# Optimization experiments

Hardware: AMD Instinct MI355X
Metric: run time of the kernel (lower is better)

Reference implementation:

```python
import jax, jax.numpy as jnp
import numpy as np

N, E, H, D_IN, D_EDGE, L = 20000, 320000, 128, 128, 32, 4
EPS = 1e-5

def setup_inputs() -> dict:
    key = jax.random.key(0)
    ks = jax.random.split(key, 16)
    d_in_edge = 2 * H + 1 + D_EDGE  # cat[h_row, h_col, radial, edge_attr] (input_nf==hidden here)
    s = 0.02
    inp = {
        'h': jax.random.normal(ks[0], (N, D_IN), jnp.float32),
        'coords': jax.random.normal(ks[1], (N, 3), jnp.float32),
        'edge_attr': jax.random.normal(ks[2], (E, D_EDGE), jnp.float32),
        'edges': jax.random.randint(ks[3], (2, E), 0, N),
        'edge_w1': jax.random.normal(ks[4], (L, d_in_edge, H), jnp.float32) * s,
        'edge_b1': jnp.zeros((L, H), jnp.float32),
        'edge_w2': jax.random.normal(ks[5], (L, H, H), jnp.float32) * s,
        'edge_b2': jnp.zeros((L, H), jnp.float32),
        'node_w1': jax.random.normal(ks[6], (L, H + H, H), jnp.float32) * s,
        'node_b1': jnp.zeros((L, H), jnp.float32),
        'node_w2': jax.random.normal(ks[7], (L, H, H), jnp.float32) * s,
        'node_b2': jnp.zeros((L, H), jnp.float32),
        'ln_g': jnp.ones((H,), jnp.float32),
        'ln_b': jnp.zeros((H,), jnp.float32),
    }
    return inp

def _egnn(h, coords, edge_attr, edges, ew1, eb1, ew2, eb2, nw1, nb1, nw2, nb2, ln_g, ln_b):
    row, col = edges[0], edges[1]
    # squared-distance radial feature; coords are not updated across layers
    # (EGNN.forward discards coordinate updates: h, _, _ = layer(...)).
    diff = coords[row] - coords[col]              # [E,3]
    radial = jnp.sum(diff * diff, axis=-1, keepdims=True)  # [E,1]
    for i in range(L):
        hr, hc = h[row], h[col]                   # gathers [E,H]
        m = jnp.concatenate([hr, hc, radial, edge_attr], axis=-1)
        m = jax.nn.silu(m @ ew1[i] + eb1[i])      # [E,H]
        m = jax.nn.silu(m @ ew2[i] + eb2[i])      # [E,H]
        agg = jax.ops.segment_sum(m, row, num_segments=N)  # scatter-add [N,H]
        z = jnp.concatenate([h, agg], axis=-1)    # [N,2H]
        out = jax.nn.silu(z @ nw1[i] + nb1[i]) @ nw2[i] + nb2[i]
        h = out if i == 0 else h + out            # layer 0 non-recurrent
    mu = jnp.mean(h, axis=-1, keepdims=True)
    var = jnp.mean((h - mu) ** 2, axis=-1, keepdims=True)
    return (h - mu) * jax.lax.rsqrt(var + EPS) * ln_g + ln_b

def reference(h, coords, edge_attr, edges, edge_w1, edge_b1, edge_w2, edge_b2,
              node_w1, node_b1, node_w2, node_b2, ln_g, ln_b):
    return _egnn(h, coords, edge_attr, edges, edge_w1, edge_b1, edge_w2, edge_b2,
                 node_w1, node_b1, node_w2, node_b2, ln_g, ln_b)
```

## Files before the change

### kernel.cpp

```cpp
#include <hip/hip_runtime.h>
#include <hip/hip_bf16.h>

#define NN 20000
#define EE 320000
#define HH 128
#define DE 32
#define LL 4

typedef __bf16 bf16_t;
typedef __bf16 bf16x8 __attribute__((ext_vector_type(8)));
typedef __bf16 bf16x4 __attribute__((ext_vector_type(4)));
typedef float f32x4 __attribute__((ext_vector_type(4)));

static __device__ __forceinline__ float silu_f(float x) {
    return x * __builtin_amdgcn_rcpf(1.f + __expf(-x));
}

static __device__ __forceinline__ int permrow(int el) {
    return ((el >> 2) & 3) * 16 + ((el >> 4) & 3) * 4 + (el & 3);
}

__global__ void prep_weights(const float* __restrict__ ew1, const float* __restrict__ eb1f,
                             const float* __restrict__ ew2,
                             const float* __restrict__ nw1, const float* __restrict__ nw2,
                             bf16_t* __restrict__ WPT, bf16_t* __restrict__ W1C,
                             bf16_t* __restrict__ W2T, bf16_t* __restrict__ N1T,
                             bf16_t* __restrict__ N2T)
{
    int i = blockIdx.x * 256 + threadIdx.x;
    const int SW = LL * 256 * 128;
    if (i < SW) {
        int l = i / (256 * 128), r = i % (256 * 128);
        int c = r / 128, k = r % 128;
        int krow = (c < 128) ? k : 128 + k;
        WPT[i] = (bf16_t)ew1[((size_t)l * 289 + krow) * 128 + (c & 127)];
        return;
    }
    i -= SW;
    const int SC = LL * 128 * 64;
    if (i < SC) {
        int l = i / (128 * 64), r = i % (128 * 64);
        int c = r / 64, kk = r % 64;
        float v;
        if (kk == 0)       v = ew1[((size_t)l * 289 + 256) * 128 + c];
        else if (kk <= 32) v = ew1[((size_t)l * 289 + 256 + kk) * 128 + c];
        else if (kk == 33) v = eb1f[l * 128 + c];
        else               v = 0.f;
        W1C[i] = (bf16_t)v;
        return;
    }
    i -= SC;
    const int S2 = LL * 128 * 128;
    if (i < S2) {
        int l = i / (128 * 128), r = i % (128 * 128);
        int n = r / 128, k = r % 128;
        W2T[i] = (bf16_t)ew2[((size_t)l * 128 + k) * 128 + n];
        return;
    }
    i -= S2;
    const int S3 = LL * 128 * 256;
    if (i < S3) {
        int l = i / (128 * 256), r = i % (128 * 256);
        int n = r / 256, k = r % 256;
        N1T[i] = (bf16_t)nw1[((size_t)l * 256 + k) * 128 + n];
        return;
    }
    i -= S3;
    if (i < S2) {
        int l = i / (128 * 128), r = i % (128 * 128);
        int n = r / 128, k = r % 128;
        N2T[i] = (bf16_t)nw2[((size_t)l * 128 + k) * 128 + n];
    }
}

__global__ void hist_kernel(const int* __restrict__ edges, int* __restrict__ counts)
{
    int e = blockIdx.x * 256 + threadIdx.x;
    if (e < EE) atomicAdd(&counts[edges[e]], 1);
}

__global__ void scan_kernel(const int* __restrict__ counts, int* __restrict__ starts)
{
    __shared__ int wsum[16];
    __shared__ int running_s;
    const int tid = threadIdx.x;
    const int lane = tid & 63, wv = tid >> 6;
    if (tid == 0) running_s = 0;
    __syncthreads();
    for (int base = 0; base < NN; base += 1024) {
        int i = base + tid;
        int v = (i < NN) ? counts[i] : 0;
        int orig = v;
        #pragma unroll
        for (int off = 1; off < 64; off <<= 1) {
            int t = __shfl_up(v, off);
            if (lane >= off) v += t;
        }
        if (lane == 63) wsum[wv] = v;
        __syncthreads();
        if (tid < 16) {
            int s = wsum[tid];
            #pragma unroll
            for (int off = 1; off < 16; off <<= 1) {
                int t = __shfl_up(s, off);
                if (tid >= off) s += t;
            }
            wsum[tid] = s;
        }
        __syncthreads();
        int waveoff = (wv == 0) ? 0 : wsum[wv - 1];
        if (i < NN) starts[i] = running_s + waveoff + v - orig;
        int total = wsum[15];
        __syncthreads();
        if (tid == 0) running_s += total;
        __syncthreads();
    }
}

__global__ void scatter_kernel(const int* __restrict__ edges, int* __restrict__ cursor,
                               int* __restrict__ eidx, int* __restrict__ row_s,
                               int* __restrict__ col_s)
{
    int e = blockIdx.x * 256 + threadIdx.x;
    if (e >= EE) return;
    int r = edges[e], c = edges[EE + e];
    int pos = atomicAdd(&cursor[r], 1);
    eidx[pos] = e;
    row_s[pos] = r;
    col_s[pos] = c;
}

__global__ void build_re(const int* __restrict__ eidx, const int* __restrict__ row_s,
                         const int* __restrict__ col_s, const float* __restrict__ coords,
                         const float* __restrict__ ea, bf16_t* __restrict__ RE)
{
    int pos = blockIdx.x * 256 + threadIdx.x;
    if (pos >= EE) return;
    int e = eidx[pos], r = row_s[pos], c = col_s[pos];
    float dx = coords[r * 3 + 0] - coords[c * 3 + 0];
    float dy = coords[r * 3 + 1] - coords[c * 3 + 1];
    float dz = coords[r * 3 + 2] - coords[c * 3 + 2];
    alignas(16) bf16_t buf[40];
    buf[0] = (bf16_t)(dx * dx + dy * dy + dz * dz);
    #pragma unroll
    for (int j = 0; j < 32; ++j) buf[1 + j] = (bf16_t)ea[(size_t)e * DE + j];
    buf[33] = (bf16_t)1.0f;
    #pragma unroll
    for (int j = 34; j < 40; ++j) buf[j] = (bf16_t)0.f;
    bf16x8* dst = (bf16x8*)(RE + (size_t)pos * 40);
    #pragma unroll
    for (int k = 0; k < 5; ++k) dst[k] = ((const bf16x8*)buf)[k];
}

__global__ __launch_bounds__(256, 2) void node_pre(
    const float* __restrict__ h, const bf16_t* __restrict__ WPT,
    bf16_t* __restrict__ P, int layer)
{
    __shared__ bf16_t Hs[64][136];
    const int tid = threadIdx.x;
    const int n0 = blockIdx.x * 64;
    {
        const int nl = tid >> 2, q = tid & 3;
        const int node = n0 + nl;
        if (node < NN) {
            const float* hp = h + (size_t)node * HH;
            #pragma unroll
            for (int j = 0; j < 8; ++j) {
                float4 v = *(const float4*)(hp + q * 32 + j * 4);
                int k = q * 32 + j * 4;
                Hs[nl][k + 0] = (bf16_t)v.x; Hs[nl][k + 1] = (bf16_t)v.y;
                Hs[nl][k + 2] = (bf16_t)v.z; Hs[nl][k + 3] = (bf16_t)v.w;
            }
        } else {
            #pragma unroll
            for (int j = 0; j < 8; ++j) {
                int k = q * 32 + j * 4;
                Hs[nl][k] = (bf16_t)0.f; Hs[nl][k + 1] = (bf16_t)0.f;
                Hs[nl][k + 2] = (bf16_t)0.f; Hs[nl][k + 3] = (bf16_t)0.f;
            }
        }
    }
    __syncthreads();

    const int lane = tid & 63, w = tid >> 6;
    const int ln = lane & 15, kg = lane >> 4;

    f32x4 acc[4][4] = {};
    const bf16_t* Wl = WPT + (size_t)layer * 256 * 128;
    #pragma unroll
    for (int kt = 0; kt < 4; ++kt) {
        const int kb = kt * 32 + kg * 8;
        bf16x8 a[4], b[4];
        #pragma unroll
        for (int m = 0; m < 4; ++m) a[m] = *(const bf16x8*)&Hs[m * 16 + ln][kb];
        #pragma unroll
        for (int n = 0; n < 4; ++n)
            b[n] = *(const bf16x8*)(Wl + (size_t)(w * 64 + n * 16 + ln) * 128 + kb);
        #pragma unroll
        for (int m = 0; m < 4; ++m)
            #pragma unroll
            for (int n = 0; n < 4; ++n)
                acc[m][n] = __builtin_amdgcn_mfma_f32_16x16x32_bf16(a[m], b[n], acc[m][n], 0, 0, 0);
    }
    #pragma unroll
    for (int n = 0; n < 4; ++n) {
        int col = w * 64 + n * 16 + ln;
        #pragma unroll
        for (int m = 0; m < 4; ++m)
            #pragma unroll
            for (int rr = 0; rr < 4; ++rr) {
                int node = n0 + m * 16 + kg * 4 + rr;
                if (node < NN) P[(size_t)node * 256 + col] = (bf16_t)acc[m][n][rr];
            }
    }
}

__global__ __launch_bounds__(256, 6) void edge_kernel(
    const bf16_t* __restrict__ P, const bf16_t* __restrict__ RE,
    const int* __restrict__ row_s, const int* __restrict__ col_s,
    const bf16_t* __restrict__ W1C, const bf16_t* __restrict__ W2T,
    const float* __restrict__ b2, float* __restrict__ agg, int layer)
{
    __shared__ bf16_t pABs[64][136];
    __shared__ bf16_t REb[64][72];

    const int tid = threadIdx.x;
    const int e0 = blockIdx.x * 64;

    {
        const int el = tid >> 2, q = tid & 3;
        const int es = e0 + permrow(el);
        const bf16_t* src = RE + (size_t)es * 40;
        bf16x8 z = {};
        if (q < 2) {
            *(bf16x8*)&REb[el][q * 16]     = *(const bf16x8*)(src + q * 16);
            *(bf16x8*)&REb[el][q * 16 + 8] = *(const bf16x8*)(src + q * 16 + 8);
        } else if (q == 2) {
            *(bf16x8*)&REb[el][32] = *(const bf16x8*)(src + 32);
            *(bf16x8*)&REb[el][40] = z;
        } else {
            *(bf16x8*)&REb[el][48] = z;
            *(bf16x8*)&REb[el][56] = z;
        }
    }
    {
        const int el = tid >> 2, q = tid & 3;
        const int es = e0 + permrow(el);
        int r = row_s[es], c = col_s[es];
        const bf16_t* pa = P + (size_t)r * 256 + q * 32;
        const bf16_t* pb = P + (size_t)c * 256 + 128 + q * 32;
        #pragma unroll
        for (int j = 0; j < 4; ++j) {
            bf16x8 va = *(const bf16x8*)(pa + j * 8);
            bf16x8 vb = *(const bf16x8*)(pb + j * 8);
            bf16x8 o;
            #pragma unroll
            for (int t = 0; t < 8; ++t) o[t] = (bf16_t)((float)va[t] + (float)vb[t]);
            *(bf16x8*)&pABs[el][q * 32 + j * 8] = o;
        }
    }
    __syncthreads();

    const int lane = tid & 63, w = tid >> 6;
    const int ln = lane & 15, kg = lane >> 4;

    f32x4 acc[4][2] = {};
    const bf16_t* W1l = W1C + (size_t)layer * 128 * 64;
    #pragma unroll
    for (int kt = 0; kt < 2; ++kt) {
        const int kb = kt * 32 + kg * 8;
        bf16x8 a[4], b[2];
        #pragma unroll
        for (int m = 0; m < 4; ++m) a[m] = *(const bf16x8*)&REb[m * 16 + ln][kb];
        #pragma unroll
        for (int n = 0; n < 2; ++n)
            b[n] = *(const bf16x8*)(W1l + (size_t)(w * 32 + n * 16 + ln) * 64 + kb);
        #pragma unroll
        for (int m = 0; m < 4; ++m)
            #pragma unroll
            for (int n = 0; n < 2; ++n)
                acc[m][n] = __builtin_amdgcn_mfma_f32_16x16x32_bf16(a[m], b[n], acc[m][n], 0, 0, 0);
    }

    #pragma unroll
    for (int n = 0; n < 2; ++n) {
        int col = w * 32 + n * 16 + ln;
        #pragma unroll
        for (int m = 0; m < 4; ++m)
            #pragma unroll
            for (int rr = 0; rr < 4; ++rr) {
                int er = m * 16 + kg * 4 + rr;
                float x = acc[m][n][rr] + (float)pABs[er][col];
                pABs[er][col] = (bf16_t)silu_f(x);
            }
    }
    __syncthreads();

    f32x4 acc2[4][2] = {};
    const bf16_t* W2l = W2T + (size_t)layer * 128 * 128;
    #pragma unroll
    for (int kt = 0; kt < 4; ++kt) {
        const int kb = kt * 32 + kg * 8;
        bf16x8 a[4], b[2];
        #pragma unroll
        for (int m = 0; m < 4; ++m) a[m] = *(const bf16x8*)&pABs[m * 16 + ln][kb];
        #pragma unroll
        for (int n = 0; n < 2; ++n)
            b[n] = *(const bf16x8*)(W2l + (size_t)(w * 32 + n * 16 + ln) * 128 + kb);
        #pragma unroll
        for (int m = 0; m < 4; ++m)
            #pragma unroll
            for (int n = 0; n < 2; ++n)
                acc2[m][n] = __builtin_amdgcn_mfma_f32_16x16x32_bf16(a[m], b[n], acc2[m][n], 0, 0, 0);
    }

    {
        int myrow[16];
        {
            const int4* rp = (const int4*)(row_s + e0 + kg * 16);
            #pragma unroll
            for (int j = 0; j < 4; ++j) {
                int4 v = rp[j];
                myrow[j * 4 + 0] = v.x; myrow[j * 4 + 1] = v.y;
                myrow[j * 4 + 2] = v.z; myrow[j * 4 + 3] = v.w;
            }
        }

        #pragma unroll
        for (int n = 0; n < 2; ++n) {
            int col = w * 32 + n * 16 + ln;
            float bias = b2[layer * 128 + col];
            float s = 0.f;
            int cur = myrow[0];
            #pragma unroll
            for (int m = 0; m < 4; ++m) {
                #pragma unroll
                for (int rr = 0; rr < 4; ++rr) {
                    int r = myrow[m * 4 + rr];
                    float v = silu_f(acc2[m][n][rr] + bias);
                    if (r != cur) {
                        atomicAdd(&agg[(size_t)cur * HH + col], s);
                        s = 0.f; cur = r;
                    }
                    s += v;
                }
            }
            atomicAdd(&agg[(size_t)cur * HH + col], s);
        }
    }
}

__global__ __launch_bounds__(256, 2) void node_fused(
    const float* __restrict__ hin, float* __restrict__ hout,
    float* __restrict__ agg,
    const bf16_t* __restrict__ N1T, const float* __restrict__ b1,
    const bf16_t* __restrict__ N2T, const float* __restrict__ b2,
    const bf16_t* __restrict__ WPT, bf16_t* __restrict__ P,
    int layer, int produceP)
{
    __shared__ bf16_t Zs[64][264];
    __shared__ bf16_t M1s[64][136];

    const int tid = threadIdx.x;
    const int n0 = blockIdx.x * 64;

    {
        const int nl = tid >> 2, q = tid & 3;
        const int node = n0 + nl;
        if (node < NN) {
            const float* hp = hin + (size_t)node * HH;
            float* ap = agg + (size_t)node * HH;
            const float4 zero4 = {0.f, 0.f, 0.f, 0.f};
            #pragma unroll
            for (int kk = 0; kk < 64; kk += 4) {
                int k = q * 64 + kk;
                float4 v;
                if (k < 128) {
                    v = *(const float4*)(hp + k);
                } else {
                    v = *(const float4*)(ap + (k - 128));
                    *(float4*)(ap + (k - 128)) = zero4;
                }
                Zs[nl][k + 0] = (bf16_t)v.x; Zs[nl][k + 1] = (bf16_t)v.y;
                Zs[nl][k + 2] = (bf16_t)v.z; Zs[nl][k + 3] = (bf16_t)v.w;
            }
        } else {
            #pragma unroll
            for (int kk = 0; kk < 64; kk += 4) {
                int k = q * 64 + kk;
                Zs[nl][k + 0] = (bf16_t)0.f; Zs[nl][k + 1] = (bf16_t)0.f;
                Zs[nl][k + 2] = (bf16_t)0.f; Zs[nl][k + 3] = (bf16_t)0.f;
            }
        }
    }
    __syncthreads();

    const int lane = tid & 63, w = tid >> 6;
    const int ln = lane & 15, kg = lane >> 4;

    f32x4 acc[2][4] = {};
    const bf16_t* N1l = N1T + (size_t)layer * 128 * 256;
    #pragma unroll
    for (int kt = 0; kt < 8; ++kt) {
        const int kb = kt * 32 + kg * 8;
        bf16x8 aW[2], bZ[4];
        #pragma unroll
        for (int oc = 0; oc < 2; ++oc)
            aW[oc] = *(const bf16x8*)(N1l + (size_t)(w * 32 + oc * 16 + ln) * 256 + kb);
        #pragma unroll
        for (int e = 0; e < 4; ++e) bZ[e] = *(const bf16x8*)&Zs[e * 16 + ln][kb];
        #pragma unroll
        for (int oc = 0; oc < 2; ++oc)
            #pragma unroll
            for (int e = 0; e < 4; ++e)
                acc[oc][e] = __builtin_amdgcn_mfma_f32_16x16x32_bf16(aW[oc], bZ[e], acc[oc][e], 0, 0, 0);
    }

    #pragma unroll
    for (int oc = 0; oc < 2; ++oc) {
        const int ob = w * 32 + oc * 16 + kg * 4;
        const float4 b14 = *(const float4*)&b1[layer * 128 + ob];
        #pragma unroll
        for (int e = 0; e < 4; ++e) {
            const int nd = e * 16 + ln;
            bf16x4 o;
            o[0] = (bf16_t)silu_f(acc[oc][e][0] + b14.x);
            o[1] = (bf16_t)silu_f(acc[oc][e][1] + b14.y);
            o[2] = (bf16_t)silu_f(acc[oc][e][2] + b14.z);
            o[3] = (bf16_t)silu_f(acc[oc][e][3] + b14.w);
            *(bf16x4*)&M1s[nd][ob] = o;
        }
    }
    __syncthreads();

    f32x4 acc2[2][4] = {};
    const bf16_t* N2l = N2T + (size_t)layer * 128 * 128;
    #pragma unroll
    for (int kt = 0; kt < 4; ++kt) {
        const int kb = kt * 32 + kg * 8;
        bf16x8 aW[2], bM[4];
        #pragma unroll
        for (int oc = 0; oc < 2; ++oc)
            aW[oc] = *(const bf16x8*)(N2l + (size_t)(w * 32 + oc * 16 + ln) * 128 + kb);
        #pragma unroll
        for (int e = 0; e < 4; ++e) bM[e] = *(const bf16x8*)&M1s[e * 16 + ln][kb];
        #pragma unroll
        for (int oc = 0; oc < 2; ++oc)
            #pragma unroll
            for (int e = 0; e < 4; ++e)
                acc2[oc][e] = __builtin_amdgcn_mfma_f32_16x16x32_bf16(aW[oc], bM[e], acc2[oc][e], 0, 0, 0);
    }

    #pragma unroll
    for (int oc = 0; oc < 2; ++oc) {
        const int ob = w * 32 + oc * 16 + kg * 4;
        const float4 b24 = *(const float4*)&b2[layer * 128 + ob];
        #pragma unroll
        for (int e = 0; e < 4; ++e) {
            const int ndl = e * 16 + ln;
            const int node = n0 + ndl;
            float x0 = acc2[oc][e][0] + b24.x;
            float x1 = acc2[oc][e][1] + b24.y;
            float x2 = acc2[oc][e][2] + b24.z;
            float x3 = acc2[oc][e][3] + b24.w;
            if (node < NN) {
                if (layer != 0) {
                    float4 hv = *(const float4*)&hin[(size_t)node * HH + ob];
                    x0 += hv.x; x1 += hv.y; x2 += hv.z; x3 += hv.w;
                }
                float4 ov; ov.x = x0; ov.y = x1; ov.z = x2; ov.w = x3;
                *(float4*)&hout[(size_t)node * HH + ob] = ov;
            }
            bf16x4 z;
            z[0] = (bf16_t)x0; z[1] = (bf16_t)x1;
            z[2] = (bf16_t)x2; z[3] = (bf16_t)x3;
            *(bf16x4*)&Zs[ndl][ob] = z;
        }
    }

    if (produceP) {
        __syncthreads();
        f32x4 accP[4][4] = {};
        const bf16_t* Wl = WPT + (size_t)(layer + 1) * 256 * 128;
        #pragma unroll
        for (int kt = 0; kt < 4; ++kt) {
            const int kb = kt * 32 + kg * 8;
            bf16x8 aW[4], bZ[4];
            #pragma unroll
            for (int oc = 0; oc < 4; ++oc)
                aW[oc] = *(const bf16x8*)(Wl + (size_t)(w * 64 + oc * 16 + ln) * 128 + kb);
            #pragma unroll
            for (int e = 0; e < 4; ++e) bZ[e] = *(const bf16x8*)&Zs[e * 16 + ln][kb];
            #pragma unroll
            for (int oc = 0; oc < 4; ++oc)
                #pragma unroll
                for (int e = 0; e < 4; ++e)
                    accP[oc][e] = __builtin_amdgcn_mfma_f32_16x16x32_bf16(aW[oc], bZ[e], accP[oc][e], 0, 0, 0);
        }
        #pragma unroll
        for (int oc = 0; oc < 4; ++oc) {
            const int pb = w * 64 + oc * 16 + kg * 4;
            #pragma unroll
            for (int e = 0; e < 4; ++e) {
                const int node = n0 + e * 16 + ln;
                if (node < NN) {
                    bf16x4 o;
                    o[0] = (bf16_t)accP[oc][e][0]; o[1] = (bf16_t)accP[oc][e][1];
                    o[2] = (bf16_t)accP[oc][e][2]; o[3] = (bf16_t)accP[oc][e][3];
                    *(bf16x4*)&P[(size_t)node * 256 + pb] = o;
                }
            }
        }
    }
}

__global__ void ln_kernel(float* __restrict__ h, const float* __restrict__ g,
                          const float* __restrict__ bb)
{
    int node = blockIdx.x * 4 + (threadIdx.x >> 6);
    int lane = threadIdx.x & 63;
    if (node >= NN) return;
    float* hp = h + (size_t)node * HH;
    float v0 = hp[lane], v1 = hp[lane + 64];
    float s = v0 + v1, sq = v0 * v0 + v1 * v1;
    #pragma unroll
    for (int o = 32; o; o >>= 1) {
        s  += __shfl_xor(s, o);
        sq += __shfl_xor(sq, o);
    }
    float mu  = s * (1.f / 128.f);
    float var = sq * (1.f / 128.f) - mu * mu;
    float inv = rsqrtf(var + 1e-5f);
    hp[lane]      = (v0 - mu) * inv * g[lane]      + bb[lane];
    hp[lane + 64] = (v1 - mu) * inv * g[lane + 64] + bb[lane + 64];
}

extern "C" void kernel_launch(void* const* d_in, const int* in_sizes, int n_in,
                              void* d_out, int out_size, void* d_ws, size_t ws_size,
                              hipStream_t stream)
{
    (void)in_sizes; (void)n_in; (void)out_size; (void)ws_size;

    const float* h_in    = (const float*)d_in[0];
    const float* coords  = (const float*)d_in[1];
    const float* ea      = (const float*)d_in[2];
    const int*   edges   = (const int*)d_in[3];
    const float* ew1     = (const float*)d_in[4];
    const float* eb1     = (const float*)d_in[5];
    const float* ew2     = (const float*)d_in[6];
    const float* eb2     = (const float*)d_in[7];
    const float* nw1     = (const float*)d_in[8];
    const float* nb1     = (const float*)d_in[9];
    const float* nw2     = (const float*)d_in[10];
    const float* nb2     = (const float*)d_in[11];
    const float* ln_g    = (const float*)d_in[12];
    const float* ln_b    = (const float*)d_in[13];

    char* ws = (char*)d_ws;
    int*    counts = (int*)(ws + 0);
    int*    starts = (int*)(ws + 80128);
    int*    cursor = (int*)(ws + 160384);
    int*    eidx   = (int*)(ws + 240512);
    int*    row_s  = (int*)(ws + 1520512);
    int*    col_s  = (int*)(ws + 2800512);
    bf16_t* RE     = (bf16_t*)(ws + 4080512);
    bf16_t* P      = (bf16_t*)(ws + 29680512);
    float*  agg    = (float*)(ws + 39920512);
    bf16_t* WPT    = (bf16_t*)(ws + 50160512);
    bf16_t* W1C    = (bf16_t*)(ws + 50422656);
    bf16_t* W2T    = (bf16_t*)(ws + 50488192);
    bf16_t* N1T    = (bf16_t*)(ws + 50619264);
    bf16_t* N2T    = (bf16_t*)(ws + 50881408);

    float* h = (float*)d_out;

    prep_weights<<<1664, 256, 0, stream>>>(ew1, eb1, ew2, nw1, nw2,
                                           WPT, W1C, W2T, N1T, N2T);

    hipMemsetAsync(counts, 0, NN * sizeof(int), stream);
    hist_kernel<<<(EE + 255) / 256, 256, 0, stream>>>(edges, counts);
    scan_kernel<<<1, 1024, 0, stream>>>(counts, starts);
    hipMemcpyAsync(cursor, starts, NN * sizeof(int),
                   hipMemcpyDeviceToDevice, stream);
    scatter_kernel<<<(EE + 255) / 256, 256, 0, stream>>>(edges, cursor, eidx, row_s, col_s);
    build_re<<<(EE + 255) / 256, 256, 0, stream>>>(eidx, row_s, col_s, coords, ea, RE);

    node_pre<<<(NN + 63) / 64, 256, 0, stream>>>(h_in, WPT, P, 0);

    hipMemsetAsync(agg, 0, (size_t)NN * HH * sizeof(float), stream);

    for (int l = 0; l < LL; ++l) {
        edge_kernel<<<EE / 64, 256, 0, stream>>>(P, RE, row_s, col_s,
                                                 W1C, W2T, eb2, agg, l);
        node_fused<<<(NN + 63) / 64, 256, 0, stream>>>(
            (l == 0) ? h_in : h, h, agg, N1T, nb1, N2T, nb2,
            WPT, P, l, (l < LL - 1) ? 1 : 0);
    }
    ln_kernel<<<NN / 4, 256, 0, stream>>>(h, ln_g, ln_b);
}
```

Baseline: 425.7 us.

## Parallelize CSR scan across blocks and fuse scatter with edge-feature build

Replaces the single-block sequential prefix scan with a multi-block local scan plus a fixup pass. The scan writes straight into the cursor array, which removes the device-to-device copy. The scatter kernel now builds the radial and edge-attr rows directly at the sorted position, which drops the eidx array and the separate build_re launch. This cuts a serialized single-block kernel, one memcpy, one launch and the eidx round-trip through memory, at the cost of writing RE at scattered positions.

```diff
diff --git a/kernel.cpp b/kernel.cpp
--- a/kernel.cpp
+++ b/kernel.cpp
@@ -79,64 +79,63 @@
     if (e < EE) atomicAdd(&counts[edges[e]], 1);
 }
 
-__global__ void scan_kernel(const int* __restrict__ counts, int* __restrict__ starts)
-{
-    __shared__ int wsum[16];
-    __shared__ int running_s;
+__global__ void scan_local(const int* __restrict__ counts, int* __restrict__ cursor,
+                           int* __restrict__ bsum)
+{
+    __shared__ int ws[16];
     const int tid = threadIdx.x;
     const int lane = tid & 63, wv = tid >> 6;
-    if (tid == 0) running_s = 0;
-    __syncthreads();
-    for (int base = 0; base < NN; base += 1024) {
-        int i = base + tid;
-        int v = (i < NN) ? counts[i] : 0;
-        int orig = v;
-        #pragma unroll
-        for (int off = 1; off < 64; off <<= 1) {
-            int t = __shfl_up(v, off);
-            if (lane >= off) v += t;
-        }
-        if (lane == 63) wsum[wv] = v;
-        __syncthreads();
-        if (tid < 16) {
-            int s = wsum[tid];
-            #pragma unroll
-            for (int off = 1; off < 16; off <<= 1) {
-                int t = __shfl_up(s, off);
-                if (tid >= off) s += t;
-            }
-            wsum[tid] = s;
-        }
-        __syncthreads();
-        int waveoff = (wv == 0) ? 0 : wsum[wv - 1];
-        if (i < NN) starts[i] = running_s + waveoff + v - orig;
-        int total = wsum[15];
-        __syncthreads();
-        if (tid == 0) running_s += total;
-        __syncthreads();
-    }
-}
-
-__global__ void scatter_kernel(const int* __restrict__ edges, int* __restrict__ cursor,
-                               int* __restrict__ eidx, int* __restrict__ row_s,
-                               int* __restrict__ col_s)
+    const int i = blockIdx.x * 1024 + tid;
+    int v = (i < NN) ? counts[i] : 0;
+    int orig = v;
+    #pragma unroll
+    for (int off = 1; off < 64; off <<= 1) {
+        int t = __shfl_up(v, off);
+        if (lane >= off) v += t;
+    }
+    if (lane == 63) ws[wv] = v;
+    __syncthreads();
+    if (tid < 16) {
+        int s = ws[tid];
+        #pragma unroll
+        for (int off = 1; off < 16; off <<= 1) {
+            int t = __shfl_up(s, off);
+            if (tid >= off) s += t;
+        }
+        ws[tid] = s;
+    }
+    __syncthreads();
+    int waveoff = (wv == 0) ? 0 : ws[wv - 1];
+    if (i < NN) cursor[i] = waveoff + v - orig;
+    if (tid == 0) bsum[blockIdx.x] = ws[15];
+}
+
+__global__ void scan_fixup(int* __restrict__ cursor, const int* __restrict__ bsum)
+{
+    __shared__ int off;
+    const int b = blockIdx.x;
+    if (threadIdx.x == 0) {
+        int s = 0;
+        for (int j = 0; j < b; ++j) s += bsum[j];
+        off = s;
+    }
+    __syncthreads();
+    if (b == 0) return;
+    int i = b * 1024 + threadIdx.x;
+    if (i < NN) cursor[i] += off;
+}
+
+__global__ void scatter_build(const int* __restrict__ edges, int* __restrict__ cursor,
+                              int* __restrict__ row_s, int* __restrict__ col_s,
+                              const float* __restrict__ coords,
+                              const float* __restrict__ ea, bf16_t* __restrict__ RE)
 {
     int e = blockIdx.x * 256 + threadIdx.x;
     if (e >= EE) return;
     int r = edges[e], c = edges[EE + e];
     int pos = atomicAdd(&cursor[r], 1);
-    eidx[pos] = e;
     row_s[pos] = r;
     col_s[pos] = c;
-}
-
-__global__ void build_re(const int* __restrict__ eidx, const int* __restrict__ row_s,
-                         const int* __restrict__ col_s, const float* __restrict__ coords,
-                         const float* __restrict__ ea, bf16_t* __restrict__ RE)
-{
-    int pos = blockIdx.x * 256 + threadIdx.x;
-    if (pos >= EE) return;
-    int e = eidx[pos], r = row_s[pos], c = col_s[pos];
     float dx = coords[r * 3 + 0] - coords[c * 3 + 0];
     float dy = coords[r * 3 + 1] - coords[c * 3 + 1];
     float dz = coords[r * 3 + 2] - coords[c * 3 + 2];
@@ -558,9 +557,8 @@
 
     char* ws = (char*)d_ws;
     int*    counts = (int*)(ws + 0);
-    int*    starts = (int*)(ws + 80128);
+    int*    bsum   = (int*)(ws + 80128);
     int*    cursor = (int*)(ws + 160384);
-    int*    eidx   = (int*)(ws + 240512);
     int*    row_s  = (int*)(ws + 1520512);
     int*    col_s  = (int*)(ws + 2800512);
     bf16_t* RE     = (bf16_t*)(ws + 4080512);
@@ -579,11 +577,10 @@
 
     hipMemsetAsync(counts, 0, NN * sizeof(int), stream);
     hist_kernel<<<(EE + 255) / 256, 256, 0, stream>>>(edges, counts);
-    scan_kernel<<<1, 1024, 0, stream>>>(counts, starts);
-    hipMemcpyAsync(cursor, starts, NN * sizeof(int),
-                   hipMemcpyDeviceToDevice, stream);
-    scatter_kernel<<<(EE + 255) / 256, 256, 0, stream>>>(edges, cursor, eidx, row_s, col_s);
-    build_re<<<(EE + 255) / 256, 256, 0, stream>>>(eidx, row_s, col_s, coords, ea, RE);
+    scan_local<<<(NN + 1023) / 1024, 1024, 0, stream>>>(counts, cursor, bsum);
+    scan_fixup<<<(NN + 1023) / 1024, 1024, 0, stream>>>(cursor, bsum);
+    scatter_build<<<(EE + 255) / 256, 256, 0, stream>>>(edges, cursor, row_s, col_s,
+                                                        coords, ea, RE);
 
     node_pre<<<(NN + 63) / 64, 256, 0, stream>>>(h_in, WPT, P, 0);
 
```

After: 395.4 us. 1.08x faster.
